# Optimization experiments

Hardware: AMD Instinct MI355X
Metric: run time of the kernel (lower is better)

## Reference

```python
import jax, jax.numpy as jnp
import numpy as np

NX = 4096
NY = 4096
DX = 0.01
DY = 0.01
DT = 0.001
CX = 1.0
CY = 1.0
CXW = DT / DX / 2.0 * CX  # 0.05, x-direction stencil coefficient
CYW = DT / DY / 2.0 * CY  # 0.05, y-direction stencil coefficient
DIAG = 1.0                # A[1,1]
NLEVEL = int(np.log2(min(NX, NY))) + 1  # 13


def _smooth(x):
    # 3x3 cross-correlation with kernel A, valid padding (stride 1, no pad).
    # A[0,1]=CYW, A[2,1]=-CYW, A[1,0]=CXW, A[1,1]=1, A[1,2]=-CXW.
    return (CYW * x[:-2, 1:-1] - CYW * x[2:, 1:-1]
            + CXW * x[1:-1, :-2] + x[1:-1, 1:-1] - CXW * x[1:-1, 2:])


def _bc(u):
    # Replicate edges (not corners: corners stay exactly 0, as in the torch code).
    H, W = u.shape
    p = jnp.zeros((H + 2, W + 2), u.dtype)
    p = p.at[1:-1, 1:-1].set(u)
    p = p.at[0, 1:-1].set(u[0])
    p = p.at[-1, 1:-1].set(u[-1])
    p = p.at[1:-1, 0].set(u[:, 0])
    p = p.at[1:-1, -1].set(u[:, -1])
    return p


def _restrict(x):
    # 2x2 average pooling, stride 2 (conv weight = 0.25 everywhere).
    return 0.25 * (x[0::2, 0::2] + x[1::2, 0::2] + x[0::2, 1::2] + x[1::2, 1::2])


def _prolong(x):
    # Nearest-neighbor upsample by 2.
    return jnp.repeat(jnp.repeat(x, 2, axis=0), 2, axis=1)


def setup_inputs() -> dict:
    key = jax.random.key(0)
    u = jax.random.normal(key, (1, 1, NY, NX), dtype=jnp.float32)
    return {"u": u, "t": 4}


def reference(u, t):
    v = u[0, 0]  # (NY, NX)
    for _ in range(t):  # t outer F-cycle iterations (b = 0 source term)
        r = _smooth(_bc(v))  # residual on finest grid, (NY, NX)
        r_s = [r]
        for _i in range(1, NLEVEL - 3):
            r = _restrict(r)
            r_s.append(r)  # coarsest stored level is 8x8
        e = jnp.zeros((1, 1), v.dtype)
        for j in reversed(range(1, NLEVEL - 3)):
            # coarse-grid correction; broadcast of (small e) + r_s[j] matches torch
            e = e - _smooth(jnp.pad(e, 1)) / DIAG + r_s[j] / DIAG
            e = _prolong(e)
        v = v - e
        v = v - _smooth(_bc(v)) / DIAG
    return v[None, None]
```

## Files before the change

kernel.cpp:

```cpp
#include <hip/hip_runtime.h>
#include <cstddef>


constexpr float CW = 0.05f;

__device__ __forceinline__ float up_val(float Pc, float Pu, float Pd, float Pl,
                                        float Pr, float rv) {
  float sm = CW * Pu - CW * Pd + CW * Pl + Pc - CW * Pr;
  return (Pc - sm) + rv;
}

__global__ __launch_bounds__(256) void k_sr_chain(
    const float* __restrict__ v, float* __restrict__ r1,
    float* __restrict__ r2, float* __restrict__ r3,
    float* __restrict__ r4, float* __restrict__ r5) {
  const int n = 4096, h = 2048;
  __shared__ float r1s[64][65];
  __shared__ float r2s[32][33];
  __shared__ float r3s[16][17];
  __shared__ float r4s[8][9];
  int tid = threadIdx.x;
  int tx = tid & 15, ty = tid >> 4;
  int bx = blockIdx.x, by = blockIdx.y;
  int g0 = 64 * by + 4 * ty;
  int h0 = 64 * bx + 4 * tx;
  int C0 = 2 * h0;
  int cl = max(C0 - 1, 0), cr = min(C0 + 8, n - 1);

  float va[4][10];
  auto loadrow = [&](int R, float* dst) {
    R = min(max(R, 0), n - 1);
    const float* row = v + (size_t)R * n;
    float4 m0 = *reinterpret_cast<const float4*>(row + C0);
    float4 m1 = *reinterpret_cast<const float4*>(row + C0 + 4);
    dst[0] = row[cl];
    dst[1] = m0.x; dst[2] = m0.y; dst[3] = m0.z; dst[4] = m0.w;
    dst[5] = m1.x; dst[6] = m1.y; dst[7] = m1.z; dst[8] = m1.w;
    dst[9] = row[cr];
  };
#pragma unroll
  for (int r = 0; r < 4; ++r) loadrow(2 * g0 - 1 + r, va[r]);

#pragma unroll
  for (int rr = 0; rr < 4; ++rr) {
    int g = g0 + rr;
    float4 o;
#pragma unroll
    for (int cc = 0; cc < 4; ++cc) {
      float s[2][2];
#pragma unroll
      for (int p = 0; p < 2; ++p)
#pragma unroll
        for (int q = 0; q < 2; ++q) {
          s[p][q] = CW * va[p][2 * cc + 1 + q] - CW * va[p + 2][2 * cc + 1 + q]
                  + CW * va[p + 1][2 * cc + q] + va[p + 1][2 * cc + 1 + q]
                  - CW * va[p + 1][2 * cc + 2 + q];
        }
      float val = 0.25f * (((s[0][0] + s[1][0]) + s[0][1]) + s[1][1]);
      (&o.x)[cc] = val;
      r1s[4 * ty + rr][4 * tx + cc] = val;
    }
    *reinterpret_cast<float4*>(r1 + (size_t)g * h + h0) = o;
    if (rr < 3) {
#pragma unroll
      for (int c = 0; c < 10; ++c) { va[0][c] = va[2][c]; va[1][c] = va[3][c]; }
      loadrow(2 * g + 3, va[2]);
      loadrow(2 * g + 4, va[3]);
    }
  }
  __syncthreads();

#pragma unroll
  for (int k = 0; k < 4; ++k) {
    int idx = tid + 256 * k;
    int I = idx >> 5, J = idx & 31;
    float val = 0.25f * (((r1s[2 * I][2 * J] + r1s[2 * I + 1][2 * J])
                          + r1s[2 * I][2 * J + 1]) + r1s[2 * I + 1][2 * J + 1]);
    r2s[I][J] = val;
    r2[(size_t)(32 * by + I) * 1024 + 32 * bx + J] = val;
  }
  __syncthreads();
  {
    int I = tid >> 4, J = tid & 15;
    float val = 0.25f * (((r2s[2 * I][2 * J] + r2s[2 * I + 1][2 * J])
                          + r2s[2 * I][2 * J + 1]) + r2s[2 * I + 1][2 * J + 1]);
    r3s[I][J] = val;
    r3[(size_t)(16 * by + I) * 512 + 16 * bx + J] = val;
  }
  __syncthreads();
  if (tid < 64) {
    int I = tid >> 3, J = tid & 7;
    float val = 0.25f * (((r3s[2 * I][2 * J] + r3s[2 * I + 1][2 * J])
                          + r3s[2 * I][2 * J + 1]) + r3s[2 * I + 1][2 * J + 1]);
    r4s[I][J] = val;
    r4[(size_t)(8 * by + I) * 256 + 8 * bx + J] = val;
  }
  __syncthreads();
  if (tid < 16) {
    int I = tid >> 2, J = tid & 3;
    float val = 0.25f * (((r4s[2 * I][2 * J] + r4s[2 * I + 1][2 * J])
                          + r4s[2 * I][2 * J + 1]) + r4s[2 * I + 1][2 * J + 1]);
    r5[(size_t)(4 * by + I) * 128 + 4 * bx + J] = val;
  }
}

__global__ __launch_bounds__(256, 1) void k_mid(
    const float* __restrict__ r5, const float* __restrict__ r4,
    const float* __restrict__ r3, const float* __restrict__ r2,
    float* __restrict__ E2) {
  __shared__ float r5s[128 * 128];
  __shared__ float r6s[64 * 64];
  __shared__ float r7s[32 * 32];
  __shared__ float r8s[16 * 16];
  __shared__ float r9s[8 * 8];
  __shared__ float E8s[16 * 16];
  __shared__ float E7s[32 * 32];
  __shared__ float E6s[64 * 64];
  __shared__ float e5r[10][128];
  __shared__ float e4s[18][20];
  __shared__ float e3s[34][35];
  int tid = threadIdx.x;
  int bx = blockIdx.x, by = blockIdx.y;

  auto up_lds = [&](const float* Ep, const float* rr, int i, int c, int nn) {
    int ss = nn >> 1;
    float Pc = Ep[(i >> 1) * ss + (c >> 1)];
    float Pu = (i > 0)      ? Ep[((i - 1) >> 1) * ss + (c >> 1)] : 0.0f;
    float Pd = (i < nn - 1) ? Ep[((i + 1) >> 1) * ss + (c >> 1)] : 0.0f;
    float Pl = (c > 0)      ? Ep[(i >> 1) * ss + ((c - 1) >> 1)] : 0.0f;
    float Pr = (c < nn - 1) ? Ep[(i >> 1) * ss + ((c + 1) >> 1)] : 0.0f;
    return up_val(Pc, Pu, Pd, Pl, Pr, rr[i * nn + c]);
  };

  for (int idx = tid; idx < 4096; idx += 256)
    reinterpret_cast<float4*>(r5s)[idx] = reinterpret_cast<const float4*>(r5)[idx];
  __syncthreads();
  for (int idx = tid; idx < 64 * 64; idx += 256) {
    int I = idx >> 6, J = idx & 63;
    float a = r5s[(2 * I) * 128 + 2 * J],     b = r5s[(2 * I + 1) * 128 + 2 * J];
    float c = r5s[(2 * I) * 128 + 2 * J + 1], d = r5s[(2 * I + 1) * 128 + 2 * J + 1];
    r6s[idx] = 0.25f * (((a + b) + c) + d);
  }
  __syncthreads();
  for (int idx = tid; idx < 32 * 32; idx += 256) {
    int I = idx >> 5, J = idx & 31;
    float a = r6s[(2 * I) * 64 + 2 * J],     b = r6s[(2 * I + 1) * 64 + 2 * J];
    float c = r6s[(2 * I) * 64 + 2 * J + 1], d = r6s[(2 * I + 1) * 64 + 2 * J + 1];
    r7s[idx] = 0.25f * (((a + b) + c) + d);
  }
  __syncthreads();
  if (tid < 16 * 16) {
    int I = tid >> 4, J = tid & 15;
    float a = r7s[(2 * I) * 32 + 2 * J],     b = r7s[(2 * I + 1) * 32 + 2 * J];
    float c = r7s[(2 * I) * 32 + 2 * J + 1], d = r7s[(2 * I + 1) * 32 + 2 * J + 1];
    r8s[tid] = 0.25f * (((a + b) + c) + d);
  }
  __syncthreads();
  if (tid < 8 * 8) {
    int I = tid >> 3, J = tid & 7;
    float a = r8s[(2 * I) * 16 + 2 * J],     b = r8s[(2 * I + 1) * 16 + 2 * J];
    float c = r8s[(2 * I) * 16 + 2 * J + 1], d = r8s[(2 * I + 1) * 16 + 2 * J + 1];
    r9s[tid] = 0.25f * (((a + b) + c) + d);
  }
  __syncthreads();
  if (tid < 16 * 16)
    E8s[tid] = up_lds(r9s, r8s, tid >> 4, tid & 15, 16);
  __syncthreads();
  if (tid < 32 * 32)
    E7s[tid] = up_lds(E8s, r7s, tid >> 5, tid & 31, 32);
  __syncthreads();
  for (int idx = tid; idx < 64 * 64; idx += 256)
    E6s[idx] = up_lds(E7s, r6s, idx >> 6, idx & 63, 64);
  __syncthreads();
  for (int idx = tid; idx < 10 * 128; idx += 256) {
    int t = idx >> 7, c = idx & 127;
    int i = min(max(8 * by - 1 + t, 0), 127);
    e5r[t][c] = up_lds(E6s, r5s, i, c, 128);
  }
  __syncthreads();
  for (int idx = tid; idx < 18 * 18; idx += 256) {
    int er = idx / 18, ec = idx % 18;
    int ga = 16 * by - 1 + er, gb = 16 * bx - 1 + ec;
    if (ga >= 0 && ga < 256 && gb >= 0 && gb < 256) {
      float Pc = e5r[(ga >> 1) - (8 * by - 1)][gb >> 1];
      float Pu = (ga > 0)   ? e5r[((ga - 1) >> 1) - (8 * by - 1)][gb >> 1] : 0.0f;
      float Pd = (ga < 255) ? e5r[((ga + 1) >> 1) - (8 * by - 1)][gb >> 1] : 0.0f;
      float Pl = (gb > 0)   ? e5r[(ga >> 1) - (8 * by - 1)][(gb - 1) >> 1] : 0.0f;
      float Pr = (gb < 255) ? e5r[(ga >> 1) - (8 * by - 1)][(gb + 1) >> 1] : 0.0f;
      e4s[er][ec] = up_val(Pc, Pu, Pd, Pl, Pr, r4[(size_t)ga * 256 + gb]);
    }
  }
  __syncthreads();
  for (int idx = tid; idx < 34 * 34; idx += 256) {
    int er = idx / 34, ec = idx % 34;
    int gr = 32 * by - 1 + er, gc = 32 * bx - 1 + ec;
    float val = 0.0f;
    if (gr >= 0 && gr < 512 && gc >= 0 && gc < 512) {
      int e4r0 = 16 * by - 1, e4c0 = 16 * bx - 1;
      float Pc = e4s[(gr >> 1) - e4r0][(gc >> 1) - e4c0];
      float Pu = (gr > 0)   ? e4s[((gr - 1) >> 1) - e4r0][(gc >> 1) - e4c0] : 0.0f;
      float Pd = (gr < 511) ? e4s[((gr + 1) >> 1) - e4r0][(gc >> 1) - e4c0] : 0.0f;
      float Pl = (gc > 0)   ? e4s[(gr >> 1) - e4r0][((gc - 1) >> 1) - e4c0] : 0.0f;
      float Pr = (gc < 511) ? e4s[(gr >> 1) - e4r0][((gc + 1) >> 1) - e4c0] : 0.0f;
      val = up_val(Pc, Pu, Pd, Pl, Pr, r3[(size_t)gr * 512 + gc]);
    }
    e3s[er][ec] = val;
  }
  __syncthreads();
  int br0 = 32 * by - 1, bc0 = 32 * bx - 1;
#pragma unroll
  for (int k = 0; k < 4; ++k) {
    int u = tid + 256 * k;
    int rr = u >> 4, f = u & 15;
    int gR = 64 * by + rr;
    int gC = 64 * bx + 4 * f;
    int rc = (gR >> 1) - br0;
    int ru = ((gR - 1) >> 1) - br0;
    int rd = ((gR + 1) >> 1) - br0;
    float4 rv = *reinterpret_cast<const float4*>(r2 + (size_t)gR * 1024 + gC);
    float4 o;
#pragma unroll
    for (int q = 0; q < 4; ++q) {
      int c = gC + q;
      int lc = (c >> 1) - bc0;
      float Pc = e3s[rc][lc];
      float Pu = (gR > 0)    ? e3s[ru][lc] : 0.0f;
      float Pd = (gR < 1023) ? e3s[rd][lc] : 0.0f;
      float Pl = (c > 0)     ? e3s[rc][((c - 1) >> 1) - bc0] : 0.0f;
      float Pr = (c < 1023)  ? e3s[rc][((c + 1) >> 1) - bc0] : 0.0f;
      (&o.x)[q] = up_val(Pc, Pu, Pd, Pl, Pr, (&rv.x)[q]);
    }
    *reinterpret_cast<float4*>(E2 + (size_t)gR * 1024 + gC) = o;
  }
}

__global__ __launch_bounds__(256) void k_up(
    const float* __restrict__ Ep, const float* __restrict__ r,
    float* __restrict__ Eo, int n) {
  int s = n >> 1;
  int j = blockIdx.x * blockDim.x + threadIdx.x;
  int i = blockIdx.y * blockDim.y + threadIdx.y;
  if (i >= s || j >= (n >> 2)) return;
  const float* ec = Ep + (size_t)i * s + 2 * j;
  float epc0 = ec[0], epc1 = ec[1];
  float epl = (j > 0) ? ec[-1] : 0.0f;
  float epr = (2 * j + 2 < s) ? ec[2] : 0.0f;
  float epu0 = 0.0f, epu1 = 0.0f, epd0 = 0.0f, epd1 = 0.0f;
  if (i > 0)     { epu0 = ec[-s]; epu1 = ec[-s + 1]; }
  if (i < s - 1) { epd0 = ec[s];  epd1 = ec[s + 1]; }
  {
    float4 rv = *reinterpret_cast<const float4*>(r + (size_t)(2 * i) * n + 4 * j);
    float4 o;
    o.x = up_val(epc0, epu0, epc0, epl,  epc0, rv.x);
    o.y = up_val(epc0, epu0, epc0, epc0, epc1, rv.y);
    o.z = up_val(epc1, epu1, epc1, epc0, epc1, rv.z);
    o.w = up_val(epc1, epu1, epc1, epc1, epr,  rv.w);
    *reinterpret_cast<float4*>(Eo + (size_t)(2 * i) * n + 4 * j) = o;
  }
  {
    float4 rv = *reinterpret_cast<const float4*>(r + (size_t)(2 * i + 1) * n + 4 * j);
    float4 o;
    o.x = up_val(epc0, epc0, epd0, epl,  epc0, rv.x);
    o.y = up_val(epc0, epc0, epd0, epc0, epc1, rv.y);
    o.z = up_val(epc1, epc1, epd1, epc0, epc1, rv.z);
    o.w = up_val(epc1, epc1, epd1, epc1, epr,  rv.w);
    *reinterpret_cast<float4*>(Eo + (size_t)(2 * i + 1) * n + 4 * j) = o;
  }
}

__global__ __launch_bounds__(256) void k_final(
    const float* __restrict__ v, const float* __restrict__ E1,
    float* __restrict__ out) {
  const int n = 4096, h = 2048;
  int J = blockIdx.x * blockDim.x + threadIdx.x;
  int i = blockIdx.y * blockDim.y + threadIdx.y;
  int c0 = 4 * J;
  int cl = max(c0 - 1, 0), cr = min(c0 + 4, n - 1);
  int ecl = cl >> 1, ecr = cr >> 1;

  float e[3][4];
  int ers0 = max(2 * i - 1, 0) >> 1;
  int ers2 = min(2 * i + 2, n - 1) >> 1;
  const int ers[3] = {ers0, i, ers2};
#pragma unroll
  for (int t = 0; t < 3; ++t) {
    const float* erow = E1 + (size_t)ers[t] * h;
    e[t][0] = erow[ecl];
    e[t][1] = erow[2 * J];
    e[t][2] = erow[2 * J + 1];
    e[t][3] = erow[ecr];
  }

  float w[4][6];
  const int tmap[4] = {0, 1, 1, 2};
#pragma unroll
  for (int rr = 0; rr < 4; ++rr) {
    int R = min(max(2 * i - 1 + rr, 0), n - 1);
    int t = tmap[rr];
    const float* vrow = v + (size_t)R * n;
    float4 m = *reinterpret_cast<const float4*>(vrow + c0);
    w[rr][0] = vrow[cl] - e[t][0];
    w[rr][1] = m.x - e[t][1];
    w[rr][2] = m.y - e[t][1];
    w[rr][3] = m.z - e[t][2];
    w[rr][4] = m.w - e[t][2];
    w[rr][5] = vrow[cr] - e[t][3];
  }
#pragma unroll
  for (int a = 0; a < 2; ++a) {
    float4 o;
#pragma unroll
    for (int qq = 0; qq < 4; ++qq) {
      float ce = w[a + 1][qq + 1];
      float sm = CW * w[a][qq + 1] - CW * w[a + 2][qq + 1]
               + CW * w[a + 1][qq] + ce - CW * w[a + 1][qq + 2];
      (&o.x)[qq] = ce - sm;
    }
    *reinterpret_cast<float4*>(out + (size_t)(2 * i + a) * n + c0) = o;
  }
}

extern "C" void kernel_launch(void* const* d_in, const int* in_sizes, int n_in,
                              void* d_out, int out_size, void* d_ws, size_t ws_size,
                              hipStream_t stream) {
  (void)in_sizes; (void)n_in; (void)out_size;
  float* u = (float*)d_in[0];
  float* out = (float*)d_out;
  char* ws = (char*)d_ws;

  size_t off = 0;
  auto alloc = [&](size_t elems) {
    float* p = (float*)(ws + off);
    off += (elems * sizeof(float) + 255) & ~(size_t)255;
    return p;
  };
  float* r1 = alloc(2048 * 2048);
  float* r2 = alloc(1024 * 1024);
  float* r3 = alloc(512 * 512);
  float* r4 = alloc(256 * 256);
  float* r5 = alloc(128 * 128);
  float* E2 = alloc(1024 * 1024);
  float* E1 = alloc(2048 * 2048);
  size_t pool = off;
  const size_t VB = (size_t)4096 * 4096 * sizeof(float);
  bool big = ws_size >= pool + VB;
  float* vws = (float*)(ws + pool);

  dim3 b(64, 4);
  auto iterate = [&](const float* vin, float* vout) {
    k_sr_chain<<<dim3(32, 32), 256, 0, stream>>>(vin, r1, r2, r3, r4, r5);
    k_mid<<<dim3(16, 16), 256, 0, stream>>>(r5, r4, r3, r2, E2);
    k_up<<<dim3(8, 256), b, 0, stream>>>(E2, r1, E1, 2048);
    k_final<<<dim3(16, 512), b, 0, stream>>>(vin, E1, vout);
  };

  if (big) {
    iterate(u, vws);
    iterate(vws, out);
    iterate(out, vws);
    iterate(vws, out);
  } else {
    iterate(u, out);
    iterate(out, u);
    iterate(u, out);
    iterate(out, u);
    hipMemcpyAsync(out, u, VB, hipMemcpyDeviceToDevice, stream);
  }
}
```

Measured before the change: 397.9 us.

## Stage residual-restrict input tile in shared memory with halved block height

```diff
diff --git a/kernel.cpp b/kernel.cpp
--- a/kernel.cpp
+++ b/kernel.cpp
@@ -10,97 +10,109 @@
   return (Pc - sm) + rv;
 }
 
+#define SR_STRIDE 133
 __global__ __launch_bounds__(256) void k_sr_chain(
     const float* __restrict__ v, float* __restrict__ r1,
     float* __restrict__ r2, float* __restrict__ r3,
     float* __restrict__ r4, float* __restrict__ r5) {
-  const int n = 4096, h = 2048;
-  __shared__ float r1s[64][65];
-  __shared__ float r2s[32][33];
-  __shared__ float r3s[16][17];
-  __shared__ float r4s[8][9];
+  const int n = 4096;
+  __shared__ float smem[66 * SR_STRIDE];
   int tid = threadIdx.x;
+  int bx = blockIdx.x, by = blockIdx.y;
+  int R0 = 64 * by - 1;
+  int C0 = 128 * bx;
+
+  for (int idx = tid; idx < 66 * 32; idx += 256) {
+    int lr = idx >> 5, k = idx & 31;
+    int gr = min(max(R0 + lr, 0), n - 1);
+    float4 m = *reinterpret_cast<const float4*>(v + (size_t)gr * n + C0 + 4 * k);
+    float* d = smem + lr * SR_STRIDE + 1 + 4 * k;
+    d[0] = m.x; d[1] = m.y; d[2] = m.z; d[3] = m.w;
+  }
+  if (tid < 132) {
+    int side = tid & 1, lr = tid >> 1;
+    int gr = min(max(R0 + lr, 0), n - 1);
+    int gc = side ? min(C0 + 128, n - 1) : max(C0 - 1, 0);
+    smem[lr * SR_STRIDE + (side ? 129 : 0)] = v[(size_t)gr * n + gc];
+  }
+  __syncthreads();
+
   int tx = tid & 15, ty = tid >> 4;
-  int bx = blockIdx.x, by = blockIdx.y;
-  int g0 = 64 * by + 4 * ty;
-  int h0 = 64 * bx + 4 * tx;
-  int C0 = 2 * h0;
-  int cl = max(C0 - 1, 0), cr = min(C0 + 8, n - 1);
-
-  float va[4][10];
-  auto loadrow = [&](int R, float* dst) {
-    R = min(max(R, 0), n - 1);
-    const float* row = v + (size_t)R * n;
-    float4 m0 = *reinterpret_cast<const float4*>(row + C0);
-    float4 m1 = *reinterpret_cast<const float4*>(row + C0 + 4);
-    dst[0] = row[cl];
-    dst[1] = m0.x; dst[2] = m0.y; dst[3] = m0.z; dst[4] = m0.w;
-    dst[5] = m1.x; dst[6] = m1.y; dst[7] = m1.z; dst[8] = m1.w;
-    dst[9] = row[cr];
-  };
-#pragma unroll
-  for (int r = 0; r < 4; ++r) loadrow(2 * g0 - 1 + r, va[r]);
-
-#pragma unroll
-  for (int rr = 0; rr < 4; ++rr) {
-    int g = g0 + rr;
-    float4 o;
-#pragma unroll
-    for (int cc = 0; cc < 4; ++cc) {
-      float s[2][2];
-#pragma unroll
-      for (int p = 0; p < 2; ++p)
-#pragma unroll
-        for (int q = 0; q < 2; ++q) {
-          s[p][q] = CW * va[p][2 * cc + 1 + q] - CW * va[p + 2][2 * cc + 1 + q]
-                  + CW * va[p + 1][2 * cc + q] + va[p + 1][2 * cc + 1 + q]
-                  - CW * va[p + 1][2 * cc + 2 + q];
-        }
-      float val = 0.25f * (((s[0][0] + s[1][0]) + s[0][1]) + s[1][1]);
-      (&o.x)[cc] = val;
-      r1s[4 * ty + rr][4 * tx + cc] = val;
-    }
-    *reinterpret_cast<float4*>(r1 + (size_t)g * h + h0) = o;
-    if (rr < 3) {
-#pragma unroll
-      for (int c = 0; c < 10; ++c) { va[0][c] = va[2][c]; va[1][c] = va[3][c]; }
-      loadrow(2 * g + 3, va[2]);
-      loadrow(2 * g + 4, va[3]);
-    }
-  }
-  __syncthreads();
-
-#pragma unroll
-  for (int k = 0; k < 4; ++k) {
+  float win[6][10];
+#pragma unroll
+  for (int rr = 0; rr < 6; ++rr) {
+    const float* row = smem + (4 * ty + rr) * SR_STRIDE + 8 * tx;
+#pragma unroll
+    for (int ww = 0; ww < 10; ++ww) win[rr][ww] = row[ww];
+  }
+  float4 ov[2];
+#pragma unroll
+  for (int oi = 0; oi < 2; ++oi) {
+#pragma unroll
+    for (int u = 0; u < 2; ++u) {
+#pragma unroll
+      for (int oj = 0; oj < 2; ++oj) {
+        float s[2][2];
+#pragma unroll
+        for (int p = 0; p < 2; ++p)
+#pragma unroll
+          for (int q = 0; q < 2; ++q) {
+            int P = 2 * oi + p, Q = 2 * oj + q;
+            s[p][q] = CW * win[P][4 * u + Q + 1] - CW * win[P + 2][4 * u + Q + 1]
+                    + CW * win[P + 1][4 * u + Q] + win[P + 1][4 * u + Q + 1]
+                    - CW * win[P + 1][4 * u + Q + 2];
+          }
+        (&ov[oi].x)[2 * u + oj] =
+            0.25f * (((s[0][0] + s[1][0]) + s[0][1]) + s[1][1]);
+      }
+    }
+    *reinterpret_cast<float4*>(
+        r1 + (size_t)(32 * by + 2 * ty + oi) * 2048 + 64 * bx + 4 * tx) = ov[oi];
+  }
+  __syncthreads();
+
+  float* r1s = smem;
+  float* r2s = smem + 32 * 65;
+  float* r3s = smem + 32 * 65 + 16 * 33;
+  float* r4s = smem + 32 * 65 + 16 * 33 + 8 * 17;
+#pragma unroll
+  for (int oi = 0; oi < 2; ++oi)
+#pragma unroll
+    for (int cc = 0; cc < 4; ++cc)
+      r1s[(2 * ty + oi) * 65 + 4 * tx + cc] = (&ov[oi].x)[cc];
+  __syncthreads();
+
+#pragma unroll
+  for (int k = 0; k < 2; ++k) {
     int idx = tid + 256 * k;
     int I = idx >> 5, J = idx & 31;
-    float val = 0.25f * (((r1s[2 * I][2 * J] + r1s[2 * I + 1][2 * J])
-                          + r1s[2 * I][2 * J + 1]) + r1s[2 * I + 1][2 * J + 1]);
-    r2s[I][J] = val;
-    r2[(size_t)(32 * by + I) * 1024 + 32 * bx + J] = val;
-  }
-  __syncthreads();
-  {
+    float val = 0.25f * (((r1s[(2 * I) * 65 + 2 * J] + r1s[(2 * I + 1) * 65 + 2 * J])
+                          + r1s[(2 * I) * 65 + 2 * J + 1]) + r1s[(2 * I + 1) * 65 + 2 * J + 1]);
+    r2s[I * 33 + J] = val;
+    r2[(size_t)(16 * by + I) * 1024 + 32 * bx + J] = val;
+  }
+  __syncthreads();
+  if (tid < 128) {
     int I = tid >> 4, J = tid & 15;
-    float val = 0.25f * (((r2s[2 * I][2 * J] + r2s[2 * I + 1][2 * J])
-                          + r2s[2 * I][2 * J + 1]) + r2s[2 * I + 1][2 * J + 1]);
-    r3s[I][J] = val;
-    r3[(size_t)(16 * by + I) * 512 + 16 * bx + J] = val;
-  }
-  __syncthreads();
-  if (tid < 64) {
+    float val = 0.25f * (((r2s[(2 * I) * 33 + 2 * J] + r2s[(2 * I + 1) * 33 + 2 * J])
+                          + r2s[(2 * I) * 33 + 2 * J + 1]) + r2s[(2 * I + 1) * 33 + 2 * J + 1]);
+    r3s[I * 17 + J] = val;
+    r3[(size_t)(8 * by + I) * 512 + 16 * bx + J] = val;
+  }
+  __syncthreads();
+  if (tid < 32) {
     int I = tid >> 3, J = tid & 7;
-    float val = 0.25f * (((r3s[2 * I][2 * J] + r3s[2 * I + 1][2 * J])
-                          + r3s[2 * I][2 * J + 1]) + r3s[2 * I + 1][2 * J + 1]);
-    r4s[I][J] = val;
-    r4[(size_t)(8 * by + I) * 256 + 8 * bx + J] = val;
-  }
-  __syncthreads();
-  if (tid < 16) {
+    float val = 0.25f * (((r3s[(2 * I) * 17 + 2 * J] + r3s[(2 * I + 1) * 17 + 2 * J])
+                          + r3s[(2 * I) * 17 + 2 * J + 1]) + r3s[(2 * I + 1) * 17 + 2 * J + 1]);
+    r4s[I * 9 + J] = val;
+    r4[(size_t)(4 * by + I) * 256 + 8 * bx + J] = val;
+  }
+  __syncthreads();
+  if (tid < 8) {
     int I = tid >> 2, J = tid & 3;
-    float val = 0.25f * (((r4s[2 * I][2 * J] + r4s[2 * I + 1][2 * J])
-                          + r4s[2 * I][2 * J + 1]) + r4s[2 * I + 1][2 * J + 1]);
-    r5[(size_t)(4 * by + I) * 128 + 4 * bx + J] = val;
+    float val = 0.25f * (((r4s[(2 * I) * 9 + 2 * J] + r4s[(2 * I + 1) * 9 + 2 * J])
+                          + r4s[(2 * I) * 9 + 2 * J + 1]) + r4s[(2 * I + 1) * 9 + 2 * J + 1]);
+    r5[(size_t)(2 * by + I) * 128 + 4 * bx + J] = val;
   }
 }
 
@@ -348,7 +360,7 @@
 
   dim3 b(64, 4);
   auto iterate = [&](const float* vin, float* vout) {
-    k_sr_chain<<<dim3(32, 32), 256, 0, stream>>>(vin, r1, r2, r3, r4, r5);
+    k_sr_chain<<<dim3(32, 64), 256, 0, stream>>>(vin, r1, r2, r3, r4, r5);
     k_mid<<<dim3(16, 16), 256, 0, stream>>>(r5, r4, r3, r2, E2);
     k_up<<<dim3(8, 256), b, 0, stream>>>(E2, r1, E1, 2048);
     k_final<<<dim3(16, 512), b, 0, stream>>>(vin, E1, vout);
```

After: 404.4 us. No clear change (+1.6%).
